# Kernel optimization log

Hardware: AMD Instinct MI355X
Metric: run time of the kernel (lower is better)

The kernel has to match this reference:

```python
import jax, jax.numpy as jnp
import numpy as np

B, S, D, H, F = 2, 4096, 768, 12, 3072
DK = D // H
EPS = 1e-6


def _ln(x, g, b):
    mu = jnp.mean(x, axis=-1, keepdims=True)
    var = jnp.mean(jnp.square(x - mu), axis=-1, keepdims=True)
    return (x - mu) * jax.lax.rsqrt(var + EPS) * g + b


def setup_inputs() -> dict:
    key = jax.random.key(0)
    ks = jax.random.split(key, 12)
    sc = 0.02
    inp = {
        "inputs_q": jax.random.normal(ks[0], (B, S, D), jnp.float32),
        "inputs_k": jax.random.normal(ks[1], (B, S, D), jnp.float32),
        "inputs_v": jax.random.normal(ks[2], (B, S, D), jnp.float32),
        "mask": jnp.ones((B, 1, 1, S), jnp.int32),
        "wq": jax.random.normal(ks[3], (D, D), jnp.float32) * sc,
        "bq": jnp.zeros((D,), jnp.float32),
        "wk": jax.random.normal(ks[4], (D, D), jnp.float32) * sc,
        "bk": jnp.zeros((D,), jnp.float32),
        "wv": jax.random.normal(ks[5], (D, D), jnp.float32) * sc,
        "bv": jnp.zeros((D,), jnp.float32),
        "wo": jax.random.normal(ks[6], (D, D), jnp.float32) * sc,
        "bo": jnp.zeros((D,), jnp.float32),
        "w1": jax.random.normal(ks[7], (D, F), jnp.float32) * sc,
        "b1": jnp.zeros((F,), jnp.float32),
        "w2": jax.random.normal(ks[8], (F, D), jnp.float32) * sc,
        "b2": jnp.zeros((D,), jnp.float32),
        "g1": jnp.ones((D,), jnp.float32),
        "be1": jnp.zeros((D,), jnp.float32),
        "g2": jnp.ones((D,), jnp.float32),
        "be2": jnp.zeros((D,), jnp.float32),
    }
    return inp


def reference(inputs_q, inputs_k, inputs_v, mask, wq, bq, wk, bk, wv, bv,
              wo, bo, w1, b1, w2, b2, g1, be1, g2, be2):
    # --- multi-head self-attention (naive, unfused as in source) ---
    q = (inputs_q @ wq + bq).reshape(B, S, H, DK).transpose(0, 2, 1, 3)  # [B,H,S,DK]
    k = (inputs_k @ wk + bk).reshape(B, S, H, DK).transpose(0, 2, 1, 3)
    v = (inputs_v @ wv + bv).reshape(B, S, H, DK).transpose(0, 2, 1, 3)
    scores = jnp.einsum("bhqd,bhkd->bhqk", q, k) / np.sqrt(DK)  # [B,H,S,S]
    scores = jnp.where(mask == 0, -jnp.inf, scores)
    attn = jax.nn.softmax(scores, axis=-1)
    ctx = jnp.einsum("bhqk,bhkd->bhqd", attn, v)
    ctx = ctx.transpose(0, 2, 1, 3).reshape(B, S, D)
    attn_out = ctx @ wo + bo
    # --- residual + LN, FFN, residual + LN (dropout p=0 -> identity) ---
    x1 = _ln(inputs_q + attn_out, g1, be1)
    ffn = jax.nn.relu(x1 @ w1 + b1) @ w2 + b2
    return _ln(x1 + ffn, g2, be2)
```

## Files before the change

kernel.cpp:

```cpp
#include <hip/hip_runtime.h>
#include <stdint.h>

#define B_ 2
#define S_ 4096
#define D_ 768
#define H_ 12
#define F_ 3072
#define DK_ 64
#define QBLK 128
#define KVB 64
#define NT (S_ / KVB)

typedef __bf16 bf16x8 __attribute__((ext_vector_type(8)));
typedef float floatx4 __attribute__((ext_vector_type(4)));
typedef float floatx16 __attribute__((ext_vector_type(16)));

__device__ __forceinline__ float bf2f(unsigned short u) {
  unsigned int x = ((unsigned int)u) << 16;
  return __builtin_bit_cast(float, x);
}
__device__ __forceinline__ unsigned short f2bf(float f) {
  unsigned int x = __builtin_bit_cast(unsigned int, f);
  x += 0x7FFFu + ((x >> 16) & 1u);
  return (unsigned short)(x >> 16);
}
__device__ __forceinline__ unsigned int cvtpk_bf16(float lo, float hi) {
  unsigned int r;
  asm("v_cvt_pk_bf16_f32 %0, %1, %2" : "=v"(r) : "v"(lo), "v"(hi));
  return r;
}

__device__ __forceinline__ void wtrans_core(const float* __restrict__ w,
                                            unsigned short* __restrict__ wt,
                                            int K, int N) {
  __shared__ float tile[32][33];
  const int n0 = blockIdx.x * 32, k0 = blockIdx.y * 32;
  const int tx = threadIdx.x & 31, ty8 = threadIdx.x >> 5;
#pragma unroll
  for (int r = 0; r < 4; r++)
    tile[ty8 + r * 8][tx] = w[(size_t)(k0 + ty8 + r * 8) * N + n0 + tx];
  __syncthreads();
#pragma unroll
  for (int r = 0; r < 4; r++)
    wt[(size_t)(n0 + ty8 + r * 8) * K + k0 + tx] = f2bf(tile[tx][ty8 + r * 8]);
}

__global__ __launch_bounds__(256) void wtrans(const float* __restrict__ w,
                                              unsigned short* __restrict__ wt,
                                              int K, int N) {
  wtrans_core(w, wt, K, N);
}

__global__ __launch_bounds__(256) void wtrans4(const float* __restrict__ w0,
                                               const float* __restrict__ w1,
                                               const float* __restrict__ w2,
                                               const float* __restrict__ w3,
                                               unsigned short* __restrict__ wtbase) {
  const int z = blockIdx.z;
  const float* w = (z == 0) ? w0 : (z == 1) ? w1 : (z == 2) ? w2 : w3;
  wtrans_core(w, wtbase + (size_t)z * 589824, 768, 768);
}

__global__ __launch_bounds__(256) void cvt_bf16_3(const float* __restrict__ x0,
                                                  const float* __restrict__ x1,
                                                  const float* __restrict__ x2,
                                                  unsigned short* __restrict__ ybase, int n8) {
  const int z = blockIdx.z;
  const float* x = (z == 0) ? x0 : (z == 1) ? x1 : x2;
  unsigned short* y = ybase + (size_t)z * 6291456;
  const int i = blockIdx.x * 256 + threadIdx.x;
  if (i >= n8) return;
  const float4 a = ((const float4*)x)[2 * i];
  const float4 b = ((const float4*)x)[2 * i + 1];
  uint4 o;
  o.x = (unsigned int)f2bf(a.x) | ((unsigned int)f2bf(a.y) << 16);
  o.y = (unsigned int)f2bf(a.z) | ((unsigned int)f2bf(a.w) << 16);
  o.z = (unsigned int)f2bf(b.x) | ((unsigned int)f2bf(b.y) << 16);
  o.w = (unsigned int)f2bf(b.z) | ((unsigned int)f2bf(b.w) << 16);
  ((uint4*)y)[i] = o;
}

template <bool RELU, int RESID_MODE, bool OUT_BF16>
__device__ __forceinline__ void gemm_core(
    const unsigned short* __restrict__ A, const unsigned short* __restrict__ Bt,
    const float* __restrict__ bias, const void* __restrict__ residv,
    void* __restrict__ outv, int M, int N, int K) {
  __shared__ __align__(16) unsigned short As[128 * 64];
  __shared__ __align__(16) unsigned short Bs[128 * 64];
  int bx = blockIdx.x, by = blockIdx.y;
  {
    const int gx = gridDim.x;
    const int nwg = gx * gridDim.y;
    const int flat = by * gx + bx;
    const int wg = (flat & 7) * (nwg >> 3) + (flat >> 3);
    bx = wg % gx; by = wg / gx;
  }
  const int t = threadIdx.x;
  const int lane = t & 63, wave = t >> 6;
  const int m0 = by * 128, n0 = bx * 128;
  const int wm = (wave >> 1) * 64, wn = (wave & 1) * 64;
  const int rl = lane & 15, kl = (lane >> 4) * 8;
  const int lrow = lane >> 3, lcol = (lane & 7) * 8;

  floatx4 zf = {0.f, 0.f, 0.f, 0.f};
  floatx4 acc[4][4];
#pragma unroll
  for (int i = 0; i < 4; i++)
#pragma unroll
    for (int j = 0; j < 4; j++) acc[i][j] = zf;

  const unsigned short* Ab = A + (size_t)(m0 + wave * 32 + lrow) * K + lcol;
  const unsigned short* Bb = Bt + (size_t)(n0 + wave * 32 + lrow) * K + lcol;
  unsigned short* AsW = As + wave * 2048;
  unsigned short* BsW = Bs + wave * 2048;

  for (int k0 = 0; k0 < K; k0 += 64) {
    __syncthreads();
#pragma unroll
    for (int ld = 0; ld < 4; ld++) {
      __builtin_amdgcn_global_load_lds(Ab + k0 + (size_t)(ld * 8) * K, AsW + ld * 512, 16, 0, 0);
      __builtin_amdgcn_global_load_lds(Bb + k0 + (size_t)(ld * 8) * K, BsW + ld * 512, 16, 0, 0);
    }
    __syncthreads();
#pragma unroll
    for (int ks = 0; ks < 2; ks++) {
      bf16x8 af[4], bff[4];
#pragma unroll
      for (int i = 0; i < 4; i++)
        af[i] = __builtin_bit_cast(bf16x8, *(const uint4*)&As[(wm + i * 16 + rl) * 64 + ks * 32 + kl]);
#pragma unroll
      for (int j = 0; j < 4; j++)
        bff[j] = __builtin_bit_cast(bf16x8, *(const uint4*)&Bs[(wn + j * 16 + rl) * 64 + ks * 32 + kl]);
#pragma unroll
      for (int i = 0; i < 4; i++)
#pragma unroll
        for (int j = 0; j < 4; j++)
          acc[i][j] = __builtin_amdgcn_mfma_f32_16x16x32_bf16(af[i], bff[j], acc[i][j], 0, 0, 0);
    }
  }

  const int r0 = (lane >> 4) * 4;
#pragma unroll
  for (int i = 0; i < 4; i++) {
#pragma unroll
    for (int j = 0; j < 4; j++) {
      const int col = n0 + wn + j * 16 + rl;
      const float bv = bias[col];
#pragma unroll
      for (int r = 0; r < 4; r++) {
        const int row = m0 + wm + i * 16 + r0 + r;
        float v = acc[i][j][r] + bv;
        if (RESID_MODE == 1) v += ((const float*)residv)[(size_t)row * N + col];
        if (RESID_MODE == 2) v += bf2f(((const unsigned short*)residv)[(size_t)row * N + col]);
        if (RELU) v = v > 0.f ? v : 0.f;
        if (OUT_BF16)
          ((unsigned short*)outv)[(size_t)row * N + col] = f2bf(v);
        else
          ((float*)outv)[(size_t)row * N + col] = v;
      }
    }
  }
}

template <bool RELU, int RESID_MODE, bool OUT_BF16>
__global__ __launch_bounds__(256, 2) void gemm_lds(
    const unsigned short* __restrict__ A, const unsigned short* __restrict__ Bt,
    const float* __restrict__ bias, const void* __restrict__ residv,
    void* __restrict__ outv, int M, int N, int K) {
  gemm_core<RELU, RESID_MODE, OUT_BF16>(A, Bt, bias, residv, outv, M, N, K);
}

__global__ __launch_bounds__(256, 2) void gemm_qkv(
    const unsigned short* __restrict__ Abase, const unsigned short* __restrict__ Btbase,
    const float* __restrict__ b0, const float* __restrict__ b1, const float* __restrict__ b2,
    unsigned short* __restrict__ outbase) {
  const int z = blockIdx.z;
  const float* bp = (z == 0) ? b0 : (z == 1) ? b1 : b2;
  gemm_core<false, 0, true>(Abase + (size_t)z * 6291456, Btbase + (size_t)z * 589824,
                            bp, nullptr, outbase + (size_t)z * 6291456, 8192, 768, 768);
}

__global__ __launch_bounds__(256, 3) void flash_attn_v5(
    const unsigned short* __restrict__ qg, const unsigned short* __restrict__ kg,
    const unsigned short* __restrict__ vg, const int* __restrict__ maskg,
    unsigned short* __restrict__ ctx) {
  __shared__ __align__(16) unsigned short Ks[2][64][64];
  __shared__ __align__(16) unsigned short Vt[2][64][64];
  __shared__ unsigned char TFlag[NT];

  const int t = threadIdx.x;
  const int L = t & 63, wv = t >> 6;
  const int q5 = L & 31, h5 = L >> 5;
  const int qb = blockIdx.x, h = blockIdx.y, b = blockIdx.z;
  const size_t bS = (size_t)b * S_;
  const int hb = h * DK_;
  const unsigned short* kbase = kg + bS * D_ + hb;
  const unsigned short* vbase = vg + bS * D_ + hb;
  const int* mp = maskg + bS;

  for (int tt = wv; tt < NT; tt += 4) {
    const int mv = mp[tt * KVB + L];
    const unsigned long long bal = __ballot(mv != 0);
    if (L == 0) TFlag[tt] = (bal == ~0ull) ? 1 : 0;
  }

  bf16x8 bq[4];
  {
    const unsigned short* qp = qg + (bS + qb * QBLK + wv * 32 + q5) * D_ + hb + h5 * 8;
#pragma unroll
    for (int ks = 0; ks < 4; ks++)
      bq[ks] = __builtin_bit_cast(bf16x8, *(const uint4*)(qp + ks * 16));
  }

  floatx16 o0, o1;
#pragma unroll
  for (int r = 0; r < 16; r++) { o0[r] = 0.f; o1[r] = 0.f; }
  float l_ = 0.f;

  const int skv = t >> 2, kc = (t & 3) * 2;
  const int cshift = q5 & 7;
  const int vsh0 = (q5 & 7) ^ (q5 >> 3);
  const int vsh1 = vsh0 ^ 4;

  uint4 kr0, kr1, vr0, vr1;
  {
    const unsigned short* kp = kbase + (size_t)skv * D_ + kc * 8;
    const unsigned short* vp = vbase + (size_t)skv * D_ + kc * 8;
    kr0 = *(const uint4*)kp; kr1 = *(const uint4*)(kp + 8);
    vr0 = *(const uint4*)vp; vr1 = *(const uint4*)(vp + 8);
    *(uint4*)&Ks[0][skv][((kc) ^ (skv & 7)) * 8] = kr0;
    *(uint4*)&Ks[0][skv][((kc + 1) ^ (skv & 7)) * 8] = kr1;
    union { uint4 u; unsigned short e[8]; } a0, a1;
    a0.u = vr0; a1.u = vr1;
#pragma unroll
    for (int e = 0; e < 8; e++) {
      const int cp0 = (((skv >> 3) ^ e ^ kc) << 3) | (skv & 7);
      const int cp1 = (((skv >> 3) ^ e ^ (kc + 1)) << 3) | (skv & 7);
      Vt[0][kc * 8 + e][cp0] = a0.e[e];
      Vt[0][kc * 8 + 8 + e][cp1] = a1.e[e];
    }
  }
  __syncthreads();

  for (int kt = 0; kt < NT; kt++) {
    const int cur = kt & 1;
    const int kv0 = kt * KVB;
    if (kt + 1 < NT) {
      const unsigned short* kp = kbase + (size_t)(kv0 + KVB + skv) * D_ + kc * 8;
      const unsigned short* vp = vbase + (size_t)(kv0 + KVB + skv) * D_ + kc * 8;
      kr0 = *(const uint4*)kp; kr1 = *(const uint4*)(kp + 8);
      vr0 = *(const uint4*)vp; vr1 = *(const uint4*)(vp + 8);
    }

    floatx16 s0, s1;
#pragma unroll
    for (int r = 0; r < 16; r++) { s0[r] = 0.f; s1[r] = 0.f; }
    __builtin_amdgcn_s_setprio(1);
#pragma unroll
    for (int ks = 0; ks < 4; ks++) {
      bf16x8 ak0 = __builtin_bit_cast(bf16x8, *(const uint4*)&Ks[cur][q5][(((ks << 1) | h5) ^ cshift) * 8]);
      bf16x8 ak1 = __builtin_bit_cast(bf16x8, *(const uint4*)&Ks[cur][32 + q5][(((ks << 1) | h5) ^ cshift) * 8]);
      s0 = __builtin_amdgcn_mfma_f32_32x32x16_bf16(ak0, bq[ks], s0, 0, 0, 0);
      s1 = __builtin_amdgcn_mfma_f32_32x32x16_bf16(ak1, bq[ks], s1, 0, 0, 0);
    }
    __builtin_amdgcn_s_setprio(0);

    const float csc = 0.180336880111120419f;
    if (TFlag[kt]) {
#pragma unroll
      for (int r = 0; r < 16; r++) {
        s0[r] = fminf(fmaxf(s0[r] * csc, -88.f), 88.f);
        s1[r] = fminf(fmaxf(s1[r] * csc, -88.f), 88.f);
      }
    } else {
#pragma unroll
      for (int r = 0; r < 16; r++) {
        const int kvl = (r & 3) + 8 * (r >> 2) + 4 * h5;
        s0[r] = fminf(fmaxf(s0[r] * csc + (mp[kv0 + kvl] ? 0.f : -1e30f), -88.f), 88.f);
        s1[r] = fminf(fmaxf(s1[r] * csc + (mp[kv0 + 32 + kvl] ? 0.f : -1e30f), -88.f), 88.f);
      }
    }
#pragma unroll
    for (int r = 0; r < 16; r++) {
      s0[r] = exp2f(s0[r]);
      s1[r] = exp2f(s1[r]);
    }
    float a8[8];
#pragma unroll
    for (int i = 0; i < 8; i++) a8[i] = (s0[i] + s0[i + 8]) + (s1[i] + s1[i + 8]);
    float lsum = ((a8[0] + a8[1]) + (a8[2] + a8[3])) + ((a8[4] + a8[5]) + (a8[6] + a8[7]));
    lsum += __shfl_xor(lsum, 32, 64);
    l_ += lsum;

    unsigned int w[16];
#pragma unroll
    for (int a = 0; a < 8; a++) {
      w[a] = cvtpk_bf16(s0[2 * a], s0[2 * a + 1]);
      w[8 + a] = cvtpk_bf16(s1[2 * a], s1[2 * a + 1]);
    }
#pragma unroll
    for (int ks = 0; ks < 4; ks++) {
      asm("v_permlane32_swap_b32 %0, %1" : "+v"(w[4 * ks]), "+v"(w[4 * ks + 2]));
      asm("v_permlane32_swap_b32 %0, %1" : "+v"(w[4 * ks + 1]), "+v"(w[4 * ks + 3]));
    }

    __builtin_amdgcn_s_setprio(1);
#pragma unroll
    for (int ks = 0; ks < 4; ks++) {
      const bf16x8 pa = __builtin_bit_cast(bf16x8,
          make_uint4(w[4 * ks], w[4 * ks + 1], w[4 * ks + 2], w[4 * ks + 3]));
      bf16x8 av0 = __builtin_bit_cast(bf16x8, *(const uint4*)&Vt[cur][q5][(((ks << 1) | h5) ^ vsh0) * 8]);
      bf16x8 av1 = __builtin_bit_cast(bf16x8, *(const uint4*)&Vt[cur][32 + q5][(((ks << 1) | h5) ^ vsh1) * 8]);
      o0 = __builtin_amdgcn_mfma_f32_32x32x16_bf16(av0, pa, o0, 0, 0, 0);
      o1 = __builtin_amdgcn_mfma_f32_32x32x16_bf16(av1, pa, o1, 0, 0, 0);
    }
    __builtin_amdgcn_s_setprio(0);

    if (kt + 1 < NT) {
      *(uint4*)&Ks[cur ^ 1][skv][((kc) ^ (skv & 7)) * 8] = kr0;
      *(uint4*)&Ks[cur ^ 1][skv][((kc + 1) ^ (skv & 7)) * 8] = kr1;
      union { uint4 u; unsigned short e[8]; } a0, a1;
      a0.u = vr0; a1.u = vr1;
#pragma unroll
      for (int e = 0; e < 8; e++) {
        const int cp0 = (((skv >> 3) ^ e ^ kc) << 3) | (skv & 7);
        const int cp1 = (((skv >> 3) ^ e ^ (kc + 1)) << 3) | (skv & 7);
        Vt[cur ^ 1][kc * 8 + e][cp0] = a0.e[e];
        Vt[cur ^ 1][kc * 8 + 8 + e][cp1] = a1.e[e];
      }
    }
    __syncthreads();
  }

  {
    const float inv = 1.f / l_;
    unsigned int ep[16];
#pragma unroll
    for (int a = 0; a < 8; a++) {
      ep[a] = cvtpk_bf16(o0[2 * a] * inv, o0[2 * a + 1] * inv);
      ep[8 + a] = cvtpk_bf16(o1[2 * a] * inv, o1[2 * a + 1] * inv);
    }
    unsigned short* crow = ctx + (bS + qb * QBLK + wv * 32 + q5) * D_ + hb;
#pragma unroll
    for (int dt = 0; dt < 2; dt++)
#pragma unroll
      for (int g4 = 0; g4 < 4; g4++)
        *(uint2*)(crow + dt * 32 + g4 * 8 + h5 * 4) =
            make_uint2(ep[dt * 8 + g4 * 2], ep[dt * 8 + g4 * 2 + 1]);
  }
}

template <bool OUT_BF16>
__global__ __launch_bounds__(256) void ln_kernel(const float* __restrict__ x,
                                                 const float* __restrict__ g,
                                                 const float* __restrict__ be,
                                                 void* __restrict__ outv) {
  __shared__ float red[4];
  const int t = threadIdx.x, lane = t & 63, wave = t >> 6;
  const size_t row = blockIdx.x;
  const float* xr = x + row * D_;
  float v0 = xr[t], v1 = xr[t + 256], v2 = xr[t + 512];
  float s = v0 + v1 + v2;
#pragma unroll
  for (int off = 32; off; off >>= 1) s += __shfl_xor(s, off, 64);
  if (lane == 0) red[wave] = s;
  __syncthreads();
  const float mu = (red[0] + red[1] + red[2] + red[3]) * (1.f / 768.f);
  __syncthreads();
  const float d0 = v0 - mu, d1 = v1 - mu, d2 = v2 - mu;
  float vs = d0 * d0 + d1 * d1 + d2 * d2;
#pragma unroll
  for (int off = 32; off; off >>= 1) vs += __shfl_xor(vs, off, 64);
  if (lane == 0) red[wave] = vs;
  __syncthreads();
  const float rs = rsqrtf((red[0] + red[1] + red[2] + red[3]) * (1.f / 768.f) + 1e-6f);
  const float r0v = d0 * rs * g[t] + be[t];
  const float r1v = d1 * rs * g[t + 256] + be[t + 256];
  const float r2v = d2 * rs * g[t + 512] + be[t + 512];
  if (OUT_BF16) {
    unsigned short* o = (unsigned short*)outv + row * D_;
    o[t] = f2bf(r0v); o[t + 256] = f2bf(r1v); o[t + 512] = f2bf(r2v);
  } else {
    float* o = (float*)outv + row * D_;
    o[t] = r0v; o[t + 256] = r1v; o[t + 512] = r2v;
  }
}

extern "C" void kernel_launch(void* const* d_in, const int* in_sizes, int n_in,
                              void* d_out, int out_size, void* d_ws, size_t ws_size,
                              hipStream_t stream) {
  const float* xq = (const float*)d_in[0];
  const float* xk = (const float*)d_in[1];
  const float* xv = (const float*)d_in[2];
  const int* mask = (const int*)d_in[3];
  const float* wq = (const float*)d_in[4];
  const float* bq = (const float*)d_in[5];
  const float* wk = (const float*)d_in[6];
  const float* bk = (const float*)d_in[7];
  const float* wv = (const float*)d_in[8];
  const float* bv = (const float*)d_in[9];
  const float* wo = (const float*)d_in[10];
  const float* bo = (const float*)d_in[11];
  const float* w1 = (const float*)d_in[12];
  const float* b1 = (const float*)d_in[13];
  const float* w2 = (const float*)d_in[14];
  const float* b2 = (const float*)d_in[15];
  const float* g1 = (const float*)d_in[16];
  const float* be1 = (const float*)d_in[17];
  const float* g2 = (const float*)d_in[18];
  const float* be2 = (const float*)d_in[19];
  float* out = (float*)d_out;
  char* ws = (char*)d_ws;

  unsigned short* WQT = (unsigned short*)(ws + 0);
  unsigned short* W1T = (unsigned short*)(ws + 4718592);
  unsigned short* W2T = (unsigned short*)(ws + 9437184);
  unsigned short* XQB = (unsigned short*)(ws + 14155776);
  unsigned short* QB = (unsigned short*)(ws + 51904512);
  unsigned short* KB = (unsigned short*)(ws + 64487424);
  unsigned short* VB = (unsigned short*)(ws + 77070336);
  unsigned short* CTXB = (unsigned short*)(ws + 14155776);
  float* X1PRE = (float*)(ws + 51904512);
  unsigned short* X1B = (unsigned short*)(ws + 77070336);
  unsigned short* HB = (unsigned short*)(ws + 14155776);
  float* X2PRE = (float*)(ws + 89653248);
  unsigned short* WOT = WQT + 3 * 589824;

  wtrans4<<<dim3(24, 24, 4), 256, 0, stream>>>(wq, wk, wv, wo, WQT);
  wtrans<<<dim3(96, 24), 256, 0, stream>>>(w1, W1T, 768, 3072);
  wtrans<<<dim3(24, 96), 256, 0, stream>>>(w2, W2T, 3072, 768);

  cvt_bf16_3<<<dim3(3072, 1, 3), 256, 0, stream>>>(xq, xk, xv, XQB, 786432);

  gemm_qkv<<<dim3(6, 64, 3), 256, 0, stream>>>(XQB, WQT, bq, bk, bv, QB);

  flash_attn_v5<<<dim3(S_ / QBLK, H_, B_), 256, 0, stream>>>(QB, KB, VB, mask, CTXB);

  gemm_lds<false, 1, false><<<dim3(6, 64), 256, 0, stream>>>(CTXB, WOT, bo, xq, X1PRE, 8192, 768, 768);

  ln_kernel<true><<<8192, 256, 0, stream>>>(X1PRE, g1, be1, X1B);

  gemm_lds<true, 0, true><<<dim3(24, 64), 256, 0, stream>>>(X1B, W1T, b1, nullptr, HB, 8192, 3072, 768);

  gemm_lds<false, 2, false><<<dim3(6, 64), 256, 0, stream>>>(HB, W2T, b2, X1B, X2PRE, 8192, 768, 3072);

  ln_kernel<false><<<8192, 256, 0, stream>>>(X2PRE, g2, be2, out);
}
```

Measured before the change: 422.5 us.

## Emit transposed V from QKV GEMM epilogue to avoid in-kernel transpose in attention

The QKV projection GEMM now writes V directly in a [B, D, S] transposed bf16 layout from its epilogue. The attention kernel loads rows of V^T with vector loads and stores them to LDS with the same XOR swizzle used for K. This replaces the per-element scattered 16-bit LDS stores that transposed V inside every KV tile iteration. The trade-off is that the GEMM epilogue for V now issues 8-byte stores strided across rows of length S, which coalesce less well.

Result: faster. 413.7 us (-2.1%).

```diff
diff --git a/kernel.cpp b/kernel.cpp
--- a/kernel.cpp
+++ b/kernel.cpp
@@ -84,7 +84,8 @@
 __device__ __forceinline__ void gemm_core(
     const unsigned short* __restrict__ A, const unsigned short* __restrict__ Bt,
     const float* __restrict__ bias, const void* __restrict__ residv,
-    void* __restrict__ outv, int M, int N, int K) {
+    void* __restrict__ outv, unsigned short* __restrict__ vtout,
+    int M, int N, int K) {
   __shared__ __align__(16) unsigned short As[128 * 64];
   __shared__ __align__(16) unsigned short Bs[128 * 64];
   int bx = blockIdx.x, by = blockIdx.y;
@@ -140,6 +141,25 @@
   }
 
   const int r0 = (lane >> 4) * 4;
+  if (vtout) {
+#pragma unroll
+    for (int i = 0; i < 4; i++) {
+#pragma unroll
+      for (int j = 0; j < 4; j++) {
+        const int col = n0 + wn + j * 16 + rl;
+        const float bv = bias[col];
+        const int rowb = m0 + wm + i * 16 + r0;
+        const int bb = rowb >> 12, s = rowb & 4095;
+        unsigned short e[4];
+#pragma unroll
+        for (int r = 0; r < 4; r++) e[r] = f2bf(acc[i][j][r] + bv);
+        *(uint2*)&vtout[((size_t)bb * D_ + col) * 4096 + s] =
+            make_uint2((unsigned int)e[0] | ((unsigned int)e[1] << 16),
+                       (unsigned int)e[2] | ((unsigned int)e[3] << 16));
+      }
+    }
+    return;
+  }
 #pragma unroll
   for (int i = 0; i < 4; i++) {
 #pragma unroll
@@ -167,22 +187,23 @@
     const unsigned short* __restrict__ A, const unsigned short* __restrict__ Bt,
     const float* __restrict__ bias, const void* __restrict__ residv,
     void* __restrict__ outv, int M, int N, int K) {
-  gemm_core<RELU, RESID_MODE, OUT_BF16>(A, Bt, bias, residv, outv, M, N, K);
+  gemm_core<RELU, RESID_MODE, OUT_BF16>(A, Bt, bias, residv, outv, nullptr, M, N, K);
 }
 
 __global__ __launch_bounds__(256, 2) void gemm_qkv(
     const unsigned short* __restrict__ Abase, const unsigned short* __restrict__ Btbase,
     const float* __restrict__ b0, const float* __restrict__ b1, const float* __restrict__ b2,
-    unsigned short* __restrict__ outbase) {
+    unsigned short* __restrict__ outbase, unsigned short* __restrict__ vtb) {
   const int z = blockIdx.z;
   const float* bp = (z == 0) ? b0 : (z == 1) ? b1 : b2;
   gemm_core<false, 0, true>(Abase + (size_t)z * 6291456, Btbase + (size_t)z * 589824,
-                            bp, nullptr, outbase + (size_t)z * 6291456, 8192, 768, 768);
-}
-
-__global__ __launch_bounds__(256, 3) void flash_attn_v5(
+                            bp, nullptr, outbase + (size_t)z * 6291456,
+                            (z == 2) ? vtb : nullptr, 8192, 768, 768);
+}
+
+__global__ __launch_bounds__(256, 3) void flash_attn_v6(
     const unsigned short* __restrict__ qg, const unsigned short* __restrict__ kg,
-    const unsigned short* __restrict__ vg, const int* __restrict__ maskg,
+    const unsigned short* __restrict__ vtg, const int* __restrict__ maskg,
     unsigned short* __restrict__ ctx) {
   __shared__ __align__(16) unsigned short Ks[2][64][64];
   __shared__ __align__(16) unsigned short Vt[2][64][64];
@@ -195,7 +216,6 @@
   const size_t bS = (size_t)b * S_;
   const int hb = h * DK_;
   const unsigned short* kbase = kg + bS * D_ + hb;
-  const unsigned short* vbase = vg + bS * D_ + hb;
   const int* mp = maskg + bS;
 
   for (int tt = wv; tt < NT; tt += 4) {
@@ -217,28 +237,19 @@
   for (int r = 0; r < 16; r++) { o0[r] = 0.f; o1[r] = 0.f; }
   float l_ = 0.f;
 
-  const int skv = t >> 2, kc = (t & 3) * 2;
+  const int srow = t >> 2, kc = (t & 3) * 2;
+  const unsigned short* vtbase = vtg + ((size_t)b * D_ + hb + srow) * 4096;
   const int cshift = q5 & 7;
-  const int vsh0 = (q5 & 7) ^ (q5 >> 3);
-  const int vsh1 = vsh0 ^ 4;
 
   uint4 kr0, kr1, vr0, vr1;
   {
-    const unsigned short* kp = kbase + (size_t)skv * D_ + kc * 8;
-    const unsigned short* vp = vbase + (size_t)skv * D_ + kc * 8;
+    const unsigned short* kp = kbase + (size_t)srow * D_ + kc * 8;
     kr0 = *(const uint4*)kp; kr1 = *(const uint4*)(kp + 8);
-    vr0 = *(const uint4*)vp; vr1 = *(const uint4*)(vp + 8);
-    *(uint4*)&Ks[0][skv][((kc) ^ (skv & 7)) * 8] = kr0;
-    *(uint4*)&Ks[0][skv][((kc + 1) ^ (skv & 7)) * 8] = kr1;
-    union { uint4 u; unsigned short e[8]; } a0, a1;
-    a0.u = vr0; a1.u = vr1;
-#pragma unroll
-    for (int e = 0; e < 8; e++) {
-      const int cp0 = (((skv >> 3) ^ e ^ kc) << 3) | (skv & 7);
-      const int cp1 = (((skv >> 3) ^ e ^ (kc + 1)) << 3) | (skv & 7);
-      Vt[0][kc * 8 + e][cp0] = a0.e[e];
-      Vt[0][kc * 8 + 8 + e][cp1] = a1.e[e];
-    }
+    vr0 = *(const uint4*)(vtbase + kc * 8); vr1 = *(const uint4*)(vtbase + kc * 8 + 8);
+    *(uint4*)&Ks[0][srow][((kc) ^ (srow & 7)) * 8] = kr0;
+    *(uint4*)&Ks[0][srow][((kc + 1) ^ (srow & 7)) * 8] = kr1;
+    *(uint4*)&Vt[0][srow][((kc) ^ (srow & 7)) * 8] = vr0;
+    *(uint4*)&Vt[0][srow][((kc + 1) ^ (srow & 7)) * 8] = vr1;
   }
   __syncthreads();
 
@@ -246,10 +257,10 @@
     const int cur = kt & 1;
     const int kv0 = kt * KVB;
     if (kt + 1 < NT) {
-      const unsigned short* kp = kbase + (size_t)(kv0 + KVB + skv) * D_ + kc * 8;
-      const unsigned short* vp = vbase + (size_t)(kv0 + KVB + skv) * D_ + kc * 8;
+      const unsigned short* kp = kbase + (size_t)(kv0 + KVB + srow) * D_ + kc * 8;
       kr0 = *(const uint4*)kp; kr1 = *(const uint4*)(kp + 8);
-      vr0 = *(const uint4*)vp; vr1 = *(const uint4*)(vp + 8);
+      vr0 = *(const uint4*)(vtbase + kv0 + KVB + kc * 8);
+      vr1 = *(const uint4*)(vtbase + kv0 + KVB + kc * 8 + 8);
     }
 
     floatx16 s0, s1;
@@ -309,25 +320,18 @@
     for (int ks = 0; ks < 4; ks++) {
       const bf16x8 pa = __builtin_bit_cast(bf16x8,
           make_uint4(w[4 * ks], w[4 * ks + 1], w[4 * ks + 2], w[4 * ks + 3]));
-      bf16x8 av0 = __builtin_bit_cast(bf16x8, *(const uint4*)&Vt[cur][q5][(((ks << 1) | h5) ^ vsh0) * 8]);
-      bf16x8 av1 = __builtin_bit_cast(bf16x8, *(const uint4*)&Vt[cur][32 + q5][(((ks << 1) | h5) ^ vsh1) * 8]);
+      bf16x8 av0 = __builtin_bit_cast(bf16x8, *(const uint4*)&Vt[cur][q5][(((ks << 1) | h5) ^ cshift) * 8]);
+      bf16x8 av1 = __builtin_bit_cast(bf16x8, *(const uint4*)&Vt[cur][32 + q5][(((ks << 1) | h5) ^ cshift) * 8]);
       o0 = __builtin_amdgcn_mfma_f32_32x32x16_bf16(av0, pa, o0, 0, 0, 0);
       o1 = __builtin_amdgcn_mfma_f32_32x32x16_bf16(av1, pa, o1, 0, 0, 0);
     }
     __builtin_amdgcn_s_setprio(0);
 
     if (kt + 1 < NT) {
-      *(uint4*)&Ks[cur ^ 1][skv][((kc) ^ (skv & 7)) * 8] = kr0;
-      *(uint4*)&Ks[cur ^ 1][skv][((kc + 1) ^ (skv & 7)) * 8] = kr1;
-      union { uint4 u; unsigned short e[8]; } a0, a1;
-      a0.u = vr0; a1.u = vr1;
-#pragma unroll
-      for (int e = 0; e < 8; e++) {
-        const int cp0 = (((skv >> 3) ^ e ^ kc) << 3) | (skv & 7);
-        const int cp1 = (((skv >> 3) ^ e ^ (kc + 1)) << 3) | (skv & 7);
-        Vt[cur ^ 1][kc * 8 + e][cp0] = a0.e[e];
-        Vt[cur ^ 1][kc * 8 + 8 + e][cp1] = a1.e[e];
-      }
+      *(uint4*)&Ks[cur ^ 1][srow][((kc) ^ (srow & 7)) * 8] = kr0;
+      *(uint4*)&Ks[cur ^ 1][srow][((kc + 1) ^ (srow & 7)) * 8] = kr1;
+      *(uint4*)&Vt[cur ^ 1][srow][((kc) ^ (srow & 7)) * 8] = vr0;
+      *(uint4*)&Vt[cur ^ 1][srow][((kc + 1) ^ (srow & 7)) * 8] = vr1;
     }
     __syncthreads();
   }
@@ -417,8 +421,7 @@
   unsigned short* W2T = (unsigned short*)(ws + 9437184);
   unsigned short* XQB = (unsigned short*)(ws + 14155776);
   unsigned short* QB = (unsigned short*)(ws + 51904512);
-  unsigned short* KB = (unsigned short*)(ws + 64487424);
-  unsigned short* VB = (unsigned short*)(ws + 77070336);
+  unsigned short* VTB = (unsigned short*)(ws + 77070336);
   unsigned short* CTXB = (unsigned short*)(ws + 14155776);
   float* X1PRE = (float*)(ws + 51904512);
   unsigned short* X1B = (unsigned short*)(ws + 77070336);
@@ -432,9 +435,9 @@
 
   cvt_bf16_3<<<dim3(3072, 1, 3), 256, 0, stream>>>(xq, xk, xv, XQB, 786432);
 
-  gemm_qkv<<<dim3(6, 64, 3), 256, 0, stream>>>(XQB, WQT, bq, bk, bv, QB);
-
-  flash_attn_v5<<<dim3(S_ / QBLK, H_, B_), 256, 0, stream>>>(QB, KB, VB, mask, CTXB);
+  gemm_qkv<<<dim3(6, 64, 3), 256, 0, stream>>>(XQB, WQT, bq, bk, bv, QB, VTB);
+
+  flash_attn_v6<<<dim3(S_ / QBLK, H_, B_), 256, 0, stream>>>(QB, QB + 6291456, VTB, mask, CTXB);
 
   gemm_lds<false, 1, false><<<dim3(6, 64), 256, 0, stream>>>(CTXB, WOT, bo, xq, X1PRE, 8192, 768, 768);
 
```
